# Optimization experiments

Measured on AMD Instinct MI355X. Metric: run time of the kernel, lower is better.

The kernel has to match this reference:

```python
import jax, jax.numpy as jnp
import numpy as np

N_NODES = 20000
N_EDGES = 640000
IN_DIM = 128
HID_DIM = 256
N_CLASSES = 3
N_TYPES = 4
N_ASPECTS = 4096


def _type_aware_gcn(x, W_type, W_self, b, src, dst, etypes, n_nodes):
    # Per-node, per-type transforms: [N, T, H]
    xt = jnp.einsum('nd,tdh->nth', x, W_type)
    # Per-edge message: transform of source node under the edge's type. [E, H]
    msg = xt[src, etypes]
    # Degree-normalized scatter-sum into destination nodes.
    agg = jax.ops.segment_sum(msg, dst, num_segments=n_nodes)
    deg = jax.ops.segment_sum(jnp.ones((src.shape[0],), dtype=x.dtype), dst,
                              num_segments=n_nodes)
    agg = agg / jnp.clip(deg, 1.0)[:, None]
    # Self-loop transform + bias.
    return agg + x @ W_self + b


def setup_inputs() -> dict:
    key = jax.random.key(0)
    ks = jax.random.split(key, 12)
    features = jax.random.normal(ks[0], (N_NODES, IN_DIM), dtype=jnp.float32)
    edge_index = jax.random.randint(ks[1], (2, N_EDGES), 0, N_NODES)
    edge_types = jax.random.randint(ks[2], (N_EDGES,), 0, N_TYPES)
    aspect_indices = jax.random.randint(ks[3], (N_ASPECTS,), 0, N_NODES)
    s1 = 1.0 / np.sqrt(IN_DIM)
    s2 = 1.0 / np.sqrt(HID_DIM)
    W_type1 = jax.random.uniform(ks[4], (N_TYPES, IN_DIM, HID_DIM), minval=-s1, maxval=s1)
    W_self1 = jax.random.uniform(ks[5], (IN_DIM, HID_DIM), minval=-s1, maxval=s1)
    b1 = jnp.zeros((HID_DIM,), dtype=jnp.float32)
    W_type2 = jax.random.uniform(ks[6], (N_TYPES, HID_DIM, HID_DIM), minval=-s2, maxval=s2)
    W_self2 = jax.random.uniform(ks[7], (HID_DIM, HID_DIM), minval=-s2, maxval=s2)
    b2 = jnp.zeros((HID_DIM,), dtype=jnp.float32)
    W_cls = jax.random.uniform(ks[8], (HID_DIM, N_CLASSES), minval=-s2, maxval=s2)
    b_cls = jnp.zeros((N_CLASSES,), dtype=jnp.float32)
    return {
        'features': features,
        'W_type1': W_type1, 'W_self1': W_self1, 'b1': b1,
        'W_type2': W_type2, 'W_self2': W_self2, 'b2': b2,
        'W_cls': W_cls, 'b_cls': b_cls,
        'edge_index': edge_index,
        'edge_types': edge_types,
        'aspect_indices': aspect_indices,
    }


def reference(features, W_type1, W_self1, b1, W_type2, W_self2, b2,
              W_cls, b_cls, edge_index, edge_types, aspect_indices):
    n = features.shape[0]
    src, dst = edge_index[0], edge_index[1]
    h = _type_aware_gcn(features, W_type1, W_self1, b1, src, dst, edge_types, n)
    h = jax.nn.relu(h)
    # dropout: eval mode -> identity
    h = _type_aware_gcn(h, W_type2, W_self2, b2, src, dst, edge_types, n)
    aspect_embeddings = h[aspect_indices]            # [A, H]
    logits = aspect_embeddings @ W_cls + b_cls       # [A, C]
    return logits
```

## Files before the change

### kernel.cpp

```cpp
#include <hip/hip_runtime.h>

#define N_NODES   20000
#define N_EDGES   640000
#define IN_DIM    128
#define HID_DIM   256
#define N_TYPES   4
#define N_ASPECTS 4096
#define NT4       (N_NODES * N_TYPES)
#define NBUCK     157
#define BCAP      5120
#define CHUNK     2560

typedef __bf16 v8bf __attribute__((ext_vector_type(8)));
typedef float  f32x4 __attribute__((ext_vector_type(4)));
typedef float  v2f   __attribute__((ext_vector_type(2)));

static __device__ __forceinline__ float bf2f(unsigned short u) {
    return __builtin_bit_cast(float, ((unsigned int)u) << 16);
}
static __device__ __forceinline__ float bflo(unsigned int u) {
    return __builtin_bit_cast(float, u << 16);
}
static __device__ __forceinline__ float bfhi(unsigned int u) {
    return __builtin_bit_cast(float, u & 0xffff0000u);
}
static __device__ __forceinline__ unsigned short f2bf(float f) {
    unsigned int u = __builtin_bit_cast(unsigned int, f);
    u += 0x7fffu + ((u >> 16) & 1u);
    return (unsigned short)(u >> 16);
}

static __device__ __forceinline__ int local_flag(const unsigned short* w, int* red) {
    int tid = threadIdx.x;
    int c = 0;
    for (int i = tid; i < 1024; i += 256) {
        unsigned hb = (w[i] >> 8) & 0x7f;
        c += (hb >= 0x39 && hb <= 0x3D) ? 1 : 0;
    }
#pragma unroll
    for (int off = 32; off >= 1; off >>= 1) c += __shfl_down(c, off);
    if ((tid & 63) == 0) red[tid >> 6] = c;
    __syncthreads();
    int tot = red[0] + red[1] + red[2] + red[3];
    __syncthreads();
    return (tot >= 768) ? 1 : 0;
}

__global__ __launch_bounds__(256) void prepA_kernel(
        const void* __restrict__ x,
        const void* __restrict__ Ws1, const void* __restrict__ Wt1,
        const void* __restrict__ Ws2, const void* __restrict__ Wt2,
        const int* __restrict__ ei, const int* __restrict__ et,
        unsigned short* __restrict__ xc,
        unsigned int* __restrict__ xc8,
        unsigned short* __restrict__ WT1,
        unsigned short* __restrict__ WT2,
        int* __restrict__ bucket_cursor,
        unsigned int* __restrict__ breg,
        int* __restrict__ flag) {
    __shared__ __align__(16) char smem[14336];
    int b = blockIdx.x, tid = threadIdx.x;
    if (b < 250) {
        unsigned int* ord = (unsigned int*)smem;
        int* hist  = (int*)(smem + 10240);
        int* start = hist + NBUCK;
        int* cur   = start + NBUCK;
        int* gbase = cur + NBUCK;
        int* sbuf  = gbase + NBUCK;
        int e0 = b * CHUNK;
        for (int i = tid; i < NBUCK; i += 256) hist[i] = 0;
        __syncthreads();
        unsigned int pk[10];
        int bk[10];
#pragma unroll
        for (int r = 0; r < 10; r++) {
            int e = e0 + r * 256 + tid;
            int s = __builtin_nontemporal_load(ei + e);
            int d = __builtin_nontemporal_load(ei + N_EDGES + e);
            int t = __builtin_nontemporal_load(et + e);
            pk[r] = (unsigned int)s | ((unsigned int)t << 15) | ((unsigned int)d << 17);
            bk[r] = d >> 7;
            atomicAdd(&hist[bk[r]], 1);
        }
        __syncthreads();
        int v = (tid < NBUCK) ? hist[tid] : 0;
        sbuf[tid] = v;
        __syncthreads();
        for (int o = 1; o < 256; o <<= 1) {
            int t = (tid >= o) ? sbuf[tid - o] : 0;
            __syncthreads();
            sbuf[tid] += t;
            __syncthreads();
        }
        if (tid < NBUCK) { start[tid] = sbuf[tid] - v; cur[tid] = sbuf[tid] - v; }
        __syncthreads();
#pragma unroll
        for (int r = 0; r < 10; r++) {
            int p = atomicAdd(&cur[bk[r]], 1);
            ord[p] = pk[r];
        }
        __syncthreads();
        for (int bb = tid; bb < NBUCK; bb += 256)
            if (hist[bb] > 0) gbase[bb] = atomicAdd(bucket_cursor + bb, hist[bb]);
        __syncthreads();
        for (int p = tid; p < CHUNK; p += 256) {
            unsigned int e = ord[p];
            int bb = (int)(e >> 24);
            int gp = gbase[bb] + (p - start[bb]);
            if (gp < BCAP)
                __builtin_nontemporal_store(e, breg + (size_t)bb * BCAP + gp);
        }
    } else if (b < 1500) {
        int bf = local_flag((const unsigned short*)Ws1, (int*)smem);
        int idx = (b - 250) * 256 + tid;
        float f[8];
        if (bf) {
            uint4 v = reinterpret_cast<const uint4*>(x)[idx];
            reinterpret_cast<uint4*>(xc)[idx] = v;
            f[0] = bflo(v.x); f[1] = bfhi(v.x);
            f[2] = bflo(v.y); f[3] = bfhi(v.y);
            f[4] = bflo(v.z); f[5] = bfhi(v.z);
            f[6] = bflo(v.w); f[7] = bfhi(v.w);
        } else {
            const float* xf = reinterpret_cast<const float*>(x) + (size_t)idx * 8;
            unsigned short r[8] __attribute__((aligned(16)));
#pragma unroll
            for (int j = 0; j < 8; j++) { f[j] = xf[j]; r[j] = f2bf(xf[j]); }
            reinterpret_cast<uint4*>(xc)[idx] = *reinterpret_cast<const uint4*>(r);
        }
        int lo = 0, hi = 0;
        lo = __builtin_amdgcn_cvt_pk_fp8_f32(f[0], f[1], lo, false);
        lo = __builtin_amdgcn_cvt_pk_fp8_f32(f[2], f[3], lo, true);
        hi = __builtin_amdgcn_cvt_pk_fp8_f32(f[4], f[5], hi, false);
        hi = __builtin_amdgcn_cvt_pk_fp8_f32(f[6], f[7], hi, true);
        xc8[idx * 2]     = (unsigned int)lo;
        xc8[idx * 2 + 1] = (unsigned int)hi;
    } else if (b < 2140) {
        int bf = local_flag((const unsigned short*)Ws1, (int*)smem);
        int idx = (b - 1500) * 256 + tid;
        int n = idx / 640, k = idx - n * 640;
        const void* p = (k < 128) ? Ws1 : Wt1;
        size_t src = (k < 128) ? ((size_t)k * 256 + n) : ((size_t)(k - 128) * 256 + n);
        WT1[idx] = bf ? ((const unsigned short*)p)[src] : f2bf(((const float*)p)[src]);
    } else if (b < 3420) {
        int bf = local_flag((const unsigned short*)Ws1, (int*)smem);
        int idx = (b - 2140) * 256 + tid;
        int n = idx / 1280, k = idx - n * 1280;
        const void* p = (k < 256) ? Ws2 : Wt2;
        size_t src = (k < 256) ? ((size_t)k * 256 + n) : ((size_t)(k - 256) * 256 + n);
        WT2[idx] = bf ? ((const unsigned short*)p)[src] : f2bf(((const float*)p)[src]);
    } else {
        int bf = local_flag((const unsigned short*)Ws1, (int*)smem);
        if (tid == 0) *flag = bf;
    }
}

__global__ __launch_bounds__(256) void bucketB_kernel(
        const unsigned int* __restrict__ breg,
        const int* __restrict__ bucket_cursor,
        unsigned short* __restrict__ perm,
        int* __restrict__ offsets4) {
    __shared__ int cnt[512], off[512];
    __shared__ int buf[256], pscan[256];
    int b = blockIdx.x, tid = threadIdx.x;
    int cv = (tid < NBUCK) ? bucket_cursor[tid] : 0;
    if (cv > BCAP) cv = BCAP;
    buf[tid] = cv;
    __syncthreads();
    for (int o = 1; o < 256; o <<= 1) {
        int t = (tid >= o) ? buf[tid - o] : 0;
        __syncthreads();
        buf[tid] += t;
        __syncthreads();
    }
    int obase = (b > 0) ? buf[b - 1] : 0;
    if (b == 0 && tid == 0) offsets4[NT4] = buf[255];
    int Eb = bucket_cursor[b];
    if (Eb > BCAP) Eb = BCAP;
    for (int i = tid; i < 512; i += 256) cnt[i] = 0;
    __syncthreads();
    const unsigned int* reg = breg + (size_t)b * BCAP;
    for (int i = tid; i < Eb; i += 256) {
        unsigned int e = reg[i];
        int seg = (((e >> 17) & 127) << 2) | ((e >> 15) & 3);
        atomicAdd(&cnt[seg], 1);
    }
    __syncthreads();
    int pv = cnt[2 * tid] + cnt[2 * tid + 1];
    pscan[tid] = pv;
    __syncthreads();
    for (int o = 1; o < 256; o <<= 1) {
        int t = (tid >= o) ? pscan[tid - o] : 0;
        __syncthreads();
        pscan[tid] += t;
        __syncthreads();
    }
    int pexcl = pscan[tid] - pv;
    off[2 * tid]     = pexcl;
    off[2 * tid + 1] = pexcl + cnt[2 * tid];
    __syncthreads();
    for (int i = tid; i < 512; i += 256) {
        int node = b * 128 + (i >> 2);
        if (node < N_NODES) offsets4[node * 4 + (i & 3)] = obase + off[i];
    }
    __syncthreads();
    for (int i = tid; i < Eb; i += 256) {
        unsigned int e = reg[i];
        int seg = (((e >> 17) & 127) << 2) | ((e >> 15) & 3);
        int p = atomicAdd(&off[seg], 1);
        perm[obase + p] = (unsigned short)(e & 0x7fff);
    }
}

template <int D>
__global__ __launch_bounds__(256) void agg8_kernel(
        const unsigned int* __restrict__ F8,
        const int* __restrict__ offs4,
        const unsigned short* __restrict__ perm,
        unsigned short* __restrict__ AG) {
    constexpr int G = D / 8;
    constexpr int NSUB = 64 / G;
    int wave = threadIdx.x >> 6, lane = threadIdx.x & 63;
    int sg = lane / G;
    int gl = lane - sg * G;
    for (int n = blockIdx.x * 4 + wave; n < N_NODES; n += gridDim.x * 4) {
        int o0 = offs4[n * 4];
        int o4 = offs4[n * 4 + 4];
        int deg = o4 - o0;
        float inv = 1.0f / (float)(deg > 1 ? deg : 1);
        int s0 = o0;
#pragma unroll
        for (int t = 0; t < 4; t++) {
            int s1 = offs4[n * 4 + t + 1];
            float a[8];
#pragma unroll
            for (int v = 0; v < 8; v++) a[v] = 0.f;
            int j = s0;
            while (j < s1) {
                int m = s1 - j;
                if (m > 64) m = 64;
                int pw = (int)perm[j + ((lane < m) ? lane : 0)];
                int nfull = (m / (NSUB * 4)) * (NSUB * 4);
                for (int base = 0; base < nfull; base += NSUB * 4) {
                    uint2 x[4];
#pragma unroll
                    for (int l = 0; l < 4; l++) {
                        int src = __shfl(pw, base + sg * 4 + l);
                        x[l] = *reinterpret_cast<const uint2*>(F8 + (size_t)src * (D / 4) + gl * 2);
                    }
#pragma unroll
                    for (int l = 0; l < 4; l++) {
                        v2f p0 = __builtin_amdgcn_cvt_pk_f32_fp8((int)x[l].x, false);
                        v2f p1 = __builtin_amdgcn_cvt_pk_f32_fp8((int)x[l].x, true);
                        v2f p2 = __builtin_amdgcn_cvt_pk_f32_fp8((int)x[l].y, false);
                        v2f p3 = __builtin_amdgcn_cvt_pk_f32_fp8((int)x[l].y, true);
                        a[0] += p0.x; a[1] += p0.y;
                        a[2] += p1.x; a[3] += p1.y;
                        a[4] += p2.x; a[5] += p2.y;
                        a[6] += p3.x; a[7] += p3.y;
                    }
                }
                for (int k = nfull; k < m; k += NSUB) {
                    int e = k + sg;
                    int valid = (e < m);
                    int idx = valid ? e : (m - 1);
                    int src = __shfl(pw, idx);
                    uint2 x = *reinterpret_cast<const uint2*>(F8 + (size_t)src * (D / 4) + gl * 2);
                    unsigned msk = valid ? 0xffffffffu : 0u;
                    x.x &= msk; x.y &= msk;
                    v2f p0 = __builtin_amdgcn_cvt_pk_f32_fp8((int)x.x, false);
                    v2f p1 = __builtin_amdgcn_cvt_pk_f32_fp8((int)x.x, true);
                    v2f p2 = __builtin_amdgcn_cvt_pk_f32_fp8((int)x.y, false);
                    v2f p3 = __builtin_amdgcn_cvt_pk_f32_fp8((int)x.y, true);
                    a[0] += p0.x; a[1] += p0.y;
                    a[2] += p1.x; a[3] += p1.y;
                    a[4] += p2.x; a[5] += p2.y;
                    a[6] += p3.x; a[7] += p3.y;
                }
                j += m;
            }
#pragma unroll
            for (int v = 0; v < 8; v++) {
                float s = a[v];
                s += __shfl_xor(s, G);
                if (NSUB == 4) s += __shfl_xor(s, 2 * G);
                a[v] = s * inv;
            }
            if (sg == 0) {
                unsigned short r[8] __attribute__((aligned(16)));
#pragma unroll
                for (int v = 0; v < 8; v++) r[v] = f2bf(a[v]);
                *reinterpret_cast<uint4*>(AG + (size_t)n * (4 * D) + t * D + gl * 8) =
                    *reinterpret_cast<const uint4*>(r);
            }
            s0 = s1;
        }
    }
}

template <int D>
__global__ __launch_bounds__(256, 6) void gemm_kernel(
        const unsigned short* __restrict__ X,
        const unsigned short* __restrict__ AG,
        const unsigned short* __restrict__ BT,
        const void* __restrict__ bias,
        const int* __restrict__ flagp,
        unsigned short* __restrict__ C,
        unsigned char* __restrict__ C8,
        int M, int relu) {
    constexpr int K = 5 * D;
    constexpr int LDW = 72;
    __shared__ __align__(16) unsigned short As[64 * LDW];
    __shared__ __align__(16) unsigned short Bs[64 * LDW];
    int b = blockIdx.x;
    int mt = (b & 7) + 8 * (b >> 5);
    int nt = (b >> 3) & 3;
    int mtiles = (M + 63) >> 6;
    if (mt >= mtiles) return;
    int m0 = mt * 64;
    int n0 = nt * 64;
    int tid  = threadIdx.x;
    int wave = tid >> 6, lane = tid & 63;
    int wm = wave >> 1, wn = wave & 1;
    int quad = lane >> 4, l16 = lane & 15;

    f32x4 acc[2][2];
#pragma unroll
    for (int i = 0; i < 2; i++)
#pragma unroll
        for (int j = 0; j < 2; j++) acc[i][j] = (f32x4){0.f, 0.f, 0.f, 0.f};

    for (int k0 = 0; k0 < K; k0 += 64) {
        const unsigned short* base = (k0 < D) ? X : AG;
        int rs  = (k0 < D) ? D : 4 * D;
        int col = (k0 < D) ? k0 : (k0 - D);
#pragma unroll
        for (int cc = 0; cc < 2; cc++) {
            int c   = tid + cc * 256;
            int row = c >> 3;
            int c8  = c & 7;
            uint4 va = make_uint4(0u, 0u, 0u, 0u);
            int gr = m0 + row;
            if (gr < M)
                va = *reinterpret_cast<const uint4*>(base + (size_t)gr * rs + col + c8 * 8);
            *reinterpret_cast<uint4*>(&As[row * LDW + c8 * 8]) = va;
            uint4 vb = *reinterpret_cast<const uint4*>(BT + (size_t)(n0 + row) * K + k0 + c8 * 8);
            *reinterpret_cast<uint4*>(&Bs[row * LDW + c8 * 8]) = vb;
        }
        __syncthreads();
#pragma unroll
        for (int ks = 0; ks < 2; ks++) {
            v8bf af[2], bfr[2];
#pragma unroll
            for (int i = 0; i < 2; i++)
                af[i] = *reinterpret_cast<const v8bf*>(
                    &As[(wm * 32 + i * 16 + l16) * LDW + ks * 32 + quad * 8]);
#pragma unroll
            for (int j = 0; j < 2; j++)
                bfr[j] = *reinterpret_cast<const v8bf*>(
                    &Bs[(wn * 32 + j * 16 + l16) * LDW + ks * 32 + quad * 8]);
#pragma unroll
            for (int i = 0; i < 2; i++)
#pragma unroll
                for (int j = 0; j < 2; j++)
                    acc[i][j] = __builtin_amdgcn_mfma_f32_16x16x32_bf16(af[i], bfr[j], acc[i][j], 0, 0, 0);
        }
        __syncthreads();
    }
    int bf = *flagp;
#pragma unroll
    for (int i = 0; i < 2; i++) {
#pragma unroll
        for (int j = 0; j < 2; j++) {
            int col = n0 + wn * 32 + j * 16 + l16;
            float bv = bf ? bf2f(((const unsigned short*)bias)[col])
                          : ((const float*)bias)[col];
#pragma unroll
            for (int r = 0; r < 4; r++) {
                int row = m0 + wm * 32 + i * 16 + quad * 4 + r;
                if (row < M) {
                    float v = acc[i][j][r] + bv;
                    if (relu) v = fmaxf(v, 0.0f);
                    C[(size_t)row * 256 + col] = f2bf(v);
                    if (C8) {
                        int pk = __builtin_amdgcn_cvt_pk_fp8_f32(v, v, 0, false);
                        C8[(size_t)row * 256 + col] = (unsigned char)(pk & 0xff);
                    }
                }
            }
        }
    }
}

__global__ void cls_kernel(const unsigned short* __restrict__ h2,
                           const int* __restrict__ aidx,
                           const void* __restrict__ Wc,
                           const void* __restrict__ bc,
                           const int* __restrict__ flagp,
                           void* __restrict__ out) {
    int lin = blockIdx.x * blockDim.x + threadIdx.x;
    int a = lin >> 6, lane = lin & 63;
    if (a >= N_ASPECTS) return;
    int bf = *flagp;
    int node = aidx[a];
    uint2 v = *reinterpret_cast<const uint2*>(h2 + (size_t)node * 256 + lane * 4);
    float hv[4] = {bflo(v.x), bfhi(v.x), bflo(v.y), bfhi(v.y)};
    float a0 = 0.f, a1 = 0.f, a2 = 0.f;
#pragma unroll
    for (int r = 0; r < 4; r++) {
        int k = lane * 4 + r;
        float w0 = bf ? bf2f(((const unsigned short*)Wc)[k * 3 + 0]) : ((const float*)Wc)[k * 3 + 0];
        float w1 = bf ? bf2f(((const unsigned short*)Wc)[k * 3 + 1]) : ((const float*)Wc)[k * 3 + 1];
        float w2 = bf ? bf2f(((const unsigned short*)Wc)[k * 3 + 2]) : ((const float*)Wc)[k * 3 + 2];
        a0 += hv[r] * w0;
        a1 += hv[r] * w1;
        a2 += hv[r] * w2;
    }
#pragma unroll
    for (int off = 32; off >= 1; off >>= 1) {
        a0 += __shfl_down(a0, off);
        a1 += __shfl_down(a1, off);
        a2 += __shfl_down(a2, off);
    }
    if (lane == 0) {
        float b0 = bf ? bf2f(((const unsigned short*)bc)[0]) : ((const float*)bc)[0];
        float b1 = bf ? bf2f(((const unsigned short*)bc)[1]) : ((const float*)bc)[1];
        float b2 = bf ? bf2f(((const unsigned short*)bc)[2]) : ((const float*)bc)[2];
        if (bf) {
            unsigned short* o = (unsigned short*)out;
            o[a * 3 + 0] = f2bf(a0 + b0);
            o[a * 3 + 1] = f2bf(a1 + b1);
            o[a * 3 + 2] = f2bf(a2 + b2);
        } else {
            float* o = (float*)out;
            o[a * 3 + 0] = a0 + b0;
            o[a * 3 + 1] = a1 + b1;
            o[a * 3 + 2] = a2 + b2;
        }
    }
}

extern "C" void kernel_launch(void* const* d_in, const int* in_sizes, int n_in,
                              void* d_out, int out_size, void* d_ws, size_t ws_size,
                              hipStream_t stream) {
    const void* x   = d_in[0];
    const void* Wt1 = d_in[1];
    const void* Ws1 = d_in[2];
    const void* b1  = d_in[3];
    const void* Wt2 = d_in[4];
    const void* Ws2 = d_in[5];
    const void* b2  = d_in[6];
    const void* Wc  = d_in[7];
    const void* bc  = d_in[8];
    const int* ei = (const int*)d_in[9];
    const int* et = (const int*)d_in[10];
    const int* ai = (const int*)d_in[11];

    char* ws = (char*)d_ws;
    size_t off = 0;
    auto alloc = [&](size_t bytes) {
        void* p = ws + off;
        off += (bytes + 255) & ~(size_t)255;
        return p;
    };
    int*            flag          = (int*)alloc(4);
    int*            bucket_cursor = (int*)alloc((size_t)NBUCK * 4);
    int*            offsets4      = (int*)alloc((size_t)(NT4 + 1) * 4);
    unsigned int*   breg          = (unsigned int*)alloc((size_t)NBUCK * BCAP * 4);
    unsigned short* perm          = (unsigned short*)alloc((size_t)N_EDGES * 2);
    unsigned short* xc            = (unsigned short*)alloc((size_t)N_NODES * IN_DIM * 2);
    unsigned int*   xc8           = (unsigned int*)alloc((size_t)N_NODES * IN_DIM);
    unsigned short* AG            = (unsigned short*)alloc((size_t)N_NODES * 4 * HID_DIM * 2);
    unsigned short* h             = (unsigned short*)alloc((size_t)N_NODES * HID_DIM * 2);
    unsigned char*  h8            = (unsigned char*)alloc((size_t)N_NODES * HID_DIM);
    unsigned short* h2            = (unsigned short*)alloc((size_t)N_NODES * HID_DIM * 2);
    unsigned short* WT1           = (unsigned short*)alloc((size_t)640 * 256 * 2);
    unsigned short* WT2           = (unsigned short*)alloc((size_t)1280 * 256 * 2);

    hipMemsetAsync(bucket_cursor, 0, (size_t)NBUCK * 4, stream);
    prepA_kernel<<<3421, 256, 0, stream>>>(x, Ws1, Wt1, Ws2, Wt2, ei, et,
                                           xc, xc8, WT1, WT2, bucket_cursor, breg, flag);
    bucketB_kernel<<<NBUCK, 256, 0, stream>>>(breg, bucket_cursor, perm, offsets4);

    agg8_kernel<IN_DIM><<<4096, 256, 0, stream>>>(xc8, offsets4, perm, AG);
    gemm_kernel<IN_DIM><<<1280, 256, 0, stream>>>(xc, AG, WT1, b1, flag, h, h8, N_NODES, 1);
    agg8_kernel<HID_DIM><<<4096, 256, 0, stream>>>((const unsigned int*)h8, offsets4, perm, AG);
    gemm_kernel<HID_DIM><<<1280, 256, 0, stream>>>(h, AG, WT2, b2, flag, h2, nullptr, N_NODES, 0);
    cls_kernel<<<(N_ASPECTS * 64) / 256, 256, 0, stream>>>(h2, ai, Wc, bc, flag, d_out);
}
```

Before: 231.4 us.

## Enlarge GEMM tiles to 128x128 and load tiles via direct global-to-LDS

The fused GEMM now uses 128x128 output tiles, with each wave computing a 64x64 sub-tile (4x4 MFMA accumulators), so operands are reused more per LDS load. Tiles are staged with global_load_lds 16-byte direct loads instead of going through registers. Rows past M are clamped to the last row rather than zero-filled. The risks are fewer blocks (320 vs 1280), possibly too few for the number of CUs, and LDS bank conflicts from the unpadded 64-wide rows.

```diff
diff --git a/kernel.cpp b/kernel.cpp
--- a/kernel.cpp
+++ b/kernel.cpp
@@ -28,6 +28,13 @@
     unsigned int u = __builtin_bit_cast(unsigned int, f);
     u += 0x7fffu + ((u >> 16) & 1u);
     return (unsigned short)(u >> 16);
+}
+
+static __device__ __forceinline__ void gload16(const unsigned short* g, unsigned short* l) {
+    __builtin_amdgcn_global_load_lds(
+        (const __attribute__((address_space(1))) void*)g,
+        (__attribute__((address_space(3))) void*)l,
+        16, 0, 0);
 }
 
 static __device__ __forceinline__ int local_flag(const unsigned short* w, int* red) {
@@ -299,7 +306,7 @@
 }
 
 template <int D>
-__global__ __launch_bounds__(256, 6) void gemm_kernel(
+__global__ __launch_bounds__(256) void gemm_kernel(
         const unsigned short* __restrict__ X,
         const unsigned short* __restrict__ AG,
         const unsigned short* __restrict__ BT,
@@ -309,75 +316,77 @@
         unsigned char* __restrict__ C8,
         int M, int relu) {
     constexpr int K = 5 * D;
-    constexpr int LDW = 72;
-    __shared__ __align__(16) unsigned short As[64 * LDW];
-    __shared__ __align__(16) unsigned short Bs[64 * LDW];
+    __shared__ __align__(16) unsigned short As[128 * 64];
+    __shared__ __align__(16) unsigned short Bs[128 * 64];
     int b = blockIdx.x;
-    int mt = (b & 7) + 8 * (b >> 5);
-    int nt = (b >> 3) & 3;
-    int mtiles = (M + 63) >> 6;
+    int mt = (b >> 4) * 8 + (b & 7);
+    int nt = (b >> 3) & 1;
+    int mtiles = (M + 127) >> 7;
     if (mt >= mtiles) return;
-    int m0 = mt * 64;
-    int n0 = nt * 64;
+    int m0 = mt * 128;
+    int n0 = nt * 128;
     int tid  = threadIdx.x;
     int wave = tid >> 6, lane = tid & 63;
     int wm = wave >> 1, wn = wave & 1;
     int quad = lane >> 4, l16 = lane & 15;
 
-    f32x4 acc[2][2];
-#pragma unroll
-    for (int i = 0; i < 2; i++)
-#pragma unroll
-        for (int j = 0; j < 2; j++) acc[i][j] = (f32x4){0.f, 0.f, 0.f, 0.f};
+    f32x4 acc[4][4];
+#pragma unroll
+    for (int i = 0; i < 4; i++)
+#pragma unroll
+        for (int j = 0; j < 4; j++) acc[i][j] = (f32x4){0.f, 0.f, 0.f, 0.f};
 
     for (int k0 = 0; k0 < K; k0 += 64) {
-        const unsigned short* base = (k0 < D) ? X : AG;
+        const unsigned short* abase = (k0 < D) ? X : AG;
         int rs  = (k0 < D) ? D : 4 * D;
         int col = (k0 < D) ? k0 : (k0 - D);
 #pragma unroll
-        for (int cc = 0; cc < 2; cc++) {
-            int c   = tid + cc * 256;
+        for (int p = 0; p < 4; p++) {
+            int c   = p * 256 + tid;
             int row = c >> 3;
             int c8  = c & 7;
-            uint4 va = make_uint4(0u, 0u, 0u, 0u);
-            int gr = m0 + row;
-            if (gr < M)
-                va = *reinterpret_cast<const uint4*>(base + (size_t)gr * rs + col + c8 * 8);
-            *reinterpret_cast<uint4*>(&As[row * LDW + c8 * 8]) = va;
-            uint4 vb = *reinterpret_cast<const uint4*>(BT + (size_t)(n0 + row) * K + k0 + c8 * 8);
-            *reinterpret_cast<uint4*>(&Bs[row * LDW + c8 * 8]) = vb;
+            int gr  = m0 + row;
+            if (gr >= M) gr = M - 1;
+            gload16(abase + (size_t)gr * rs + col + c8 * 8, &As[c * 8]);
+        }
+#pragma unroll
+        for (int p = 0; p < 4; p++) {
+            int c   = p * 256 + tid;
+            int row = c >> 3;
+            int c8  = c & 7;
+            gload16(BT + (size_t)(n0 + row) * K + k0 + c8 * 8, &Bs[c * 8]);
         }
         __syncthreads();
 #pragma unroll
         for (int ks = 0; ks < 2; ks++) {
-            v8bf af[2], bfr[2];
-#pragma unroll
-            for (int i = 0; i < 2; i++)
+            v8bf af[4], bfr[4];
+#pragma unroll
+            for (int i = 0; i < 4; i++)
                 af[i] = *reinterpret_cast<const v8bf*>(
-                    &As[(wm * 32 + i * 16 + l16) * LDW + ks * 32 + quad * 8]);
-#pragma unroll
-            for (int j = 0; j < 2; j++)
+                    &As[(wm * 64 + i * 16 + l16) * 64 + ks * 32 + quad * 8]);
+#pragma unroll
+            for (int j = 0; j < 4; j++)
                 bfr[j] = *reinterpret_cast<const v8bf*>(
-                    &Bs[(wn * 32 + j * 16 + l16) * LDW + ks * 32 + quad * 8]);
-#pragma unroll
-            for (int i = 0; i < 2; i++)
-#pragma unroll
-                for (int j = 0; j < 2; j++)
+                    &Bs[(wn * 64 + j * 16 + l16) * 64 + ks * 32 + quad * 8]);
+#pragma unroll
+            for (int i = 0; i < 4; i++)
+#pragma unroll
+                for (int j = 0; j < 4; j++)
                     acc[i][j] = __builtin_amdgcn_mfma_f32_16x16x32_bf16(af[i], bfr[j], acc[i][j], 0, 0, 0);
         }
         __syncthreads();
     }
     int bf = *flagp;
 #pragma unroll
-    for (int i = 0; i < 2; i++) {
-#pragma unroll
-        for (int j = 0; j < 2; j++) {
-            int col = n0 + wn * 32 + j * 16 + l16;
+    for (int i = 0; i < 4; i++) {
+#pragma unroll
+        for (int j = 0; j < 4; j++) {
+            int col = n0 + wn * 64 + j * 16 + l16;
             float bv = bf ? bf2f(((const unsigned short*)bias)[col])
                           : ((const float*)bias)[col];
 #pragma unroll
             for (int r = 0; r < 4; r++) {
-                int row = m0 + wm * 32 + i * 16 + quad * 4 + r;
+                int row = m0 + wm * 64 + i * 16 + quad * 4 + r;
                 if (row < M) {
                     float v = acc[i][j][r] + bv;
                     if (relu) v = fmaxf(v, 0.0f);
@@ -483,8 +492,8 @@
     bucketB_kernel<<<NBUCK, 256, 0, stream>>>(breg, bucket_cursor, perm, offsets4);
 
     agg8_kernel<IN_DIM><<<4096, 256, 0, stream>>>(xc8, offsets4, perm, AG);
-    gemm_kernel<IN_DIM><<<1280, 256, 0, stream>>>(xc, AG, WT1, b1, flag, h, h8, N_NODES, 1);
+    gemm_kernel<IN_DIM><<<320, 256, 0, stream>>>(xc, AG, WT1, b1, flag, h, h8, N_NODES, 1);
     agg8_kernel<HID_DIM><<<4096, 256, 0, stream>>>((const unsigned int*)h8, offsets4, perm, AG);
-    gemm_kernel<HID_DIM><<<1280, 256, 0, stream>>>(h, AG, WT2, b2, flag, h2, nullptr, N_NODES, 0);
+    gemm_kernel<HID_DIM><<<320, 256, 0, stream>>>(h, AG, WT2, b2, flag, h2, nullptr, N_NODES, 0);
     cls_kernel<<<(N_ASPECTS * 64) / 256, 256, 0, stream>>>(h2, ai, Wc, bc, flag, d_out);
 }
```

Result: slower. 244.4 us (+5.6%).

## Fuse all GCN stages into one cooperative persistent kernel with grid syncs

Applied to the files above, without the earlier changes.

Wraps the prep, bucketing, both aggregation passes, both GEMMs and the classifier into one cooperative mega-kernel. Each stage runs its former blocks as virtual blocks in a grid-stride loop, and stages are separated by grid-wide syncs. The memset is replaced by an in-kernel zeroing step. The aim is to remove the launch gaps and tail effects between seven kernels plus a memset. The cost is that the fused kernel's register use and shared memory now set the occupancy for every stage, the GEMM loses its explicit occupancy hint, and each grid barrier adds its own overhead; a multi-kernel fallback is kept for when the cooperative launch fails.

```diff
diff --git a/kernel.cpp b/kernel.cpp
--- a/kernel.cpp
+++ b/kernel.cpp
@@ -1,4 +1,5 @@
 #include <hip/hip_runtime.h>
+#include <hip/hip_cooperative_groups.h>
 
 #define N_NODES   20000
 #define N_EDGES   640000
@@ -10,10 +11,28 @@
 #define NBUCK     157
 #define BCAP      5120
 #define CHUNK     2560
+#define GEMM_VB   1280
+#define CLS_VB    ((N_ASPECTS * 64) / 256)
 
 typedef __bf16 v8bf __attribute__((ext_vector_type(8)));
 typedef float  f32x4 __attribute__((ext_vector_type(4)));
 typedef float  v2f   __attribute__((ext_vector_type(2)));
+
+struct P {
+    const void *x, *Ws1, *Wt1, *Ws2, *Wt2, *b1, *b2, *Wc, *bc;
+    const int *ei, *et, *ai;
+    unsigned short *xc;
+    unsigned int *xc8;
+    unsigned short *WT1, *WT2;
+    int *bucket_cursor;
+    unsigned int *breg;
+    int *flag;
+    unsigned short *perm;
+    int *offsets4;
+    unsigned short *AG, *h, *h2;
+    unsigned char *h8;
+    void *out;
+};
 
 static __device__ __forceinline__ float bf2f(unsigned short u) {
     return __builtin_bit_cast(float, ((unsigned int)u) << 16);
@@ -46,20 +65,8 @@
     return (tot >= 768) ? 1 : 0;
 }
 
-__global__ __launch_bounds__(256) void prepA_kernel(
-        const void* __restrict__ x,
-        const void* __restrict__ Ws1, const void* __restrict__ Wt1,
-        const void* __restrict__ Ws2, const void* __restrict__ Wt2,
-        const int* __restrict__ ei, const int* __restrict__ et,
-        unsigned short* __restrict__ xc,
-        unsigned int* __restrict__ xc8,
-        unsigned short* __restrict__ WT1,
-        unsigned short* __restrict__ WT2,
-        int* __restrict__ bucket_cursor,
-        unsigned int* __restrict__ breg,
-        int* __restrict__ flag) {
-    __shared__ __align__(16) char smem[14336];
-    int b = blockIdx.x, tid = threadIdx.x;
+static __device__ void prepA_vb(const P& p, int b, char* smem) {
+    int tid = threadIdx.x;
     if (b < 250) {
         unsigned int* ord = (unsigned int*)smem;
         int* hist  = (int*)(smem + 10240);
@@ -75,9 +82,9 @@
 #pragma unroll
         for (int r = 0; r < 10; r++) {
             int e = e0 + r * 256 + tid;
-            int s = __builtin_nontemporal_load(ei + e);
-            int d = __builtin_nontemporal_load(ei + N_EDGES + e);
-            int t = __builtin_nontemporal_load(et + e);
+            int s = __builtin_nontemporal_load(p.ei + e);
+            int d = __builtin_nontemporal_load(p.ei + N_EDGES + e);
+            int t = __builtin_nontemporal_load(p.et + e);
             pk[r] = (unsigned int)s | ((unsigned int)t << 15) | ((unsigned int)d << 17);
             bk[r] = d >> 7;
             atomicAdd(&hist[bk[r]], 1);
@@ -96,74 +103,73 @@
         __syncthreads();
 #pragma unroll
         for (int r = 0; r < 10; r++) {
-            int p = atomicAdd(&cur[bk[r]], 1);
-            ord[p] = pk[r];
+            int pp = atomicAdd(&cur[bk[r]], 1);
+            ord[pp] = pk[r];
         }
         __syncthreads();
         for (int bb = tid; bb < NBUCK; bb += 256)
-            if (hist[bb] > 0) gbase[bb] = atomicAdd(bucket_cursor + bb, hist[bb]);
-        __syncthreads();
-        for (int p = tid; p < CHUNK; p += 256) {
-            unsigned int e = ord[p];
+            if (hist[bb] > 0) gbase[bb] = atomicAdd(p.bucket_cursor + bb, hist[bb]);
+        __syncthreads();
+        for (int pp = tid; pp < CHUNK; pp += 256) {
+            unsigned int e = ord[pp];
             int bb = (int)(e >> 24);
-            int gp = gbase[bb] + (p - start[bb]);
+            int gp = gbase[bb] + (pp - start[bb]);
             if (gp < BCAP)
-                __builtin_nontemporal_store(e, breg + (size_t)bb * BCAP + gp);
-        }
+                __builtin_nontemporal_store(e, p.breg + (size_t)bb * BCAP + gp);
+        }
+        __syncthreads();
     } else if (b < 1500) {
-        int bf = local_flag((const unsigned short*)Ws1, (int*)smem);
+        int bf = local_flag((const unsigned short*)p.Ws1, (int*)smem);
         int idx = (b - 250) * 256 + tid;
         float f[8];
         if (bf) {
-            uint4 v = reinterpret_cast<const uint4*>(x)[idx];
-            reinterpret_cast<uint4*>(xc)[idx] = v;
+            uint4 v = reinterpret_cast<const uint4*>(p.x)[idx];
+            reinterpret_cast<uint4*>(p.xc)[idx] = v;
             f[0] = bflo(v.x); f[1] = bfhi(v.x);
             f[2] = bflo(v.y); f[3] = bfhi(v.y);
             f[4] = bflo(v.z); f[5] = bfhi(v.z);
             f[6] = bflo(v.w); f[7] = bfhi(v.w);
         } else {
-            const float* xf = reinterpret_cast<const float*>(x) + (size_t)idx * 8;
+            const float* xf = reinterpret_cast<const float*>(p.x) + (size_t)idx * 8;
             unsigned short r[8] __attribute__((aligned(16)));
 #pragma unroll
             for (int j = 0; j < 8; j++) { f[j] = xf[j]; r[j] = f2bf(xf[j]); }
-            reinterpret_cast<uint4*>(xc)[idx] = *reinterpret_cast<const uint4*>(r);
+            reinterpret_cast<uint4*>(p.xc)[idx] = *reinterpret_cast<const uint4*>(r);
         }
         int lo = 0, hi = 0;
         lo = __builtin_amdgcn_cvt_pk_fp8_f32(f[0], f[1], lo, false);
         lo = __builtin_amdgcn_cvt_pk_fp8_f32(f[2], f[3], lo, true);
         hi = __builtin_amdgcn_cvt_pk_fp8_f32(f[4], f[5], hi, false);
         hi = __builtin_amdgcn_cvt_pk_fp8_f32(f[6], f[7], hi, true);
-        xc8[idx * 2]     = (unsigned int)lo;
-        xc8[idx * 2 + 1] = (unsigned int)hi;
+        p.xc8[idx * 2]     = (unsigned int)lo;
+        p.xc8[idx * 2 + 1] = (unsigned int)hi;
     } else if (b < 2140) {
-        int bf = local_flag((const unsigned short*)Ws1, (int*)smem);
+        int bf = local_flag((const unsigned short*)p.Ws1, (int*)smem);
         int idx = (b - 1500) * 256 + tid;
         int n = idx / 640, k = idx - n * 640;
-        const void* p = (k < 128) ? Ws1 : Wt1;
+        const void* q = (k < 128) ? p.Ws1 : p.Wt1;
         size_t src = (k < 128) ? ((size_t)k * 256 + n) : ((size_t)(k - 128) * 256 + n);
-        WT1[idx] = bf ? ((const unsigned short*)p)[src] : f2bf(((const float*)p)[src]);
+        p.WT1[idx] = bf ? ((const unsigned short*)q)[src] : f2bf(((const float*)q)[src]);
     } else if (b < 3420) {
-        int bf = local_flag((const unsigned short*)Ws1, (int*)smem);
+        int bf = local_flag((const unsigned short*)p.Ws1, (int*)smem);
         int idx = (b - 2140) * 256 + tid;
         int n = idx / 1280, k = idx - n * 1280;
-        const void* p = (k < 256) ? Ws2 : Wt2;
+        const void* q = (k < 256) ? p.Ws2 : p.Wt2;
         size_t src = (k < 256) ? ((size_t)k * 256 + n) : ((size_t)(k - 256) * 256 + n);
-        WT2[idx] = bf ? ((const unsigned short*)p)[src] : f2bf(((const float*)p)[src]);
+        p.WT2[idx] = bf ? ((const unsigned short*)q)[src] : f2bf(((const float*)q)[src]);
     } else {
-        int bf = local_flag((const unsigned short*)Ws1, (int*)smem);
-        if (tid == 0) *flag = bf;
-    }
-}
-
-__global__ __launch_bounds__(256) void bucketB_kernel(
-        const unsigned int* __restrict__ breg,
-        const int* __restrict__ bucket_cursor,
-        unsigned short* __restrict__ perm,
-        int* __restrict__ offsets4) {
-    __shared__ int cnt[512], off[512];
-    __shared__ int buf[256], pscan[256];
-    int b = blockIdx.x, tid = threadIdx.x;
-    int cv = (tid < NBUCK) ? bucket_cursor[tid] : 0;
+        int bf = local_flag((const unsigned short*)p.Ws1, (int*)smem);
+        if (tid == 0) *p.flag = bf;
+    }
+}
+
+static __device__ void bucketB_vb(const P& p, int b, char* smem) {
+    int* cnt   = (int*)smem;
+    int* off   = cnt + 512;
+    int* buf   = off + 512;
+    int* pscan = buf + 256;
+    int tid = threadIdx.x;
+    int cv = (tid < NBUCK) ? p.bucket_cursor[tid] : 0;
     if (cv > BCAP) cv = BCAP;
     buf[tid] = cv;
     __syncthreads();
@@ -174,12 +180,12 @@
         __syncthreads();
     }
     int obase = (b > 0) ? buf[b - 1] : 0;
-    if (b == 0 && tid == 0) offsets4[NT4] = buf[255];
-    int Eb = bucket_cursor[b];
+    if (b == 0 && tid == 0) p.offsets4[NT4] = buf[255];
+    int Eb = p.bucket_cursor[b];
     if (Eb > BCAP) Eb = BCAP;
     for (int i = tid; i < 512; i += 256) cnt[i] = 0;
     __syncthreads();
-    const unsigned int* reg = breg + (size_t)b * BCAP;
+    const unsigned int* reg = p.breg + (size_t)b * BCAP;
     for (int i = tid; i < Eb; i += 256) {
         unsigned int e = reg[i];
         int seg = (((e >> 17) & 127) << 2) | ((e >> 15) & 3);
@@ -201,23 +207,23 @@
     __syncthreads();
     for (int i = tid; i < 512; i += 256) {
         int node = b * 128 + (i >> 2);
-        if (node < N_NODES) offsets4[node * 4 + (i & 3)] = obase + off[i];
+        if (node < N_NODES) p.offsets4[node * 4 + (i & 3)] = obase + off[i];
     }
     __syncthreads();
     for (int i = tid; i < Eb; i += 256) {
         unsigned int e = reg[i];
         int seg = (((e >> 17) & 127) << 2) | ((e >> 15) & 3);
-        int p = atomicAdd(&off[seg], 1);
-        perm[obase + p] = (unsigned short)(e & 0x7fff);
-    }
+        int pp = atomicAdd(&off[seg], 1);
+        p.perm[obase + pp] = (unsigned short)(e & 0x7fff);
+    }
+    __syncthreads();
 }
 
 template <int D>
-__global__ __launch_bounds__(256) void agg8_kernel(
-        const unsigned int* __restrict__ F8,
-        const int* __restrict__ offs4,
-        const unsigned short* __restrict__ perm,
-        unsigned short* __restrict__ AG) {
+static __device__ void agg8_body(const unsigned int* __restrict__ F8,
+                                 const int* __restrict__ offs4,
+                                 const unsigned short* __restrict__ perm,
+                                 unsigned short* __restrict__ AG) {
     constexpr int G = D / 8;
     constexpr int NSUB = 64 / G;
     int wave = threadIdx.x >> 6, lane = threadIdx.x & 63;
@@ -242,18 +248,18 @@
                 int pw = (int)perm[j + ((lane < m) ? lane : 0)];
                 int nfull = (m / (NSUB * 4)) * (NSUB * 4);
                 for (int base = 0; base < nfull; base += NSUB * 4) {
-                    uint2 x[4];
+                    uint2 xv[4];
 #pragma unroll
                     for (int l = 0; l < 4; l++) {
                         int src = __shfl(pw, base + sg * 4 + l);
-                        x[l] = *reinterpret_cast<const uint2*>(F8 + (size_t)src * (D / 4) + gl * 2);
+                        xv[l] = *reinterpret_cast<const uint2*>(F8 + (size_t)src * (D / 4) + gl * 2);
                     }
 #pragma unroll
                     for (int l = 0; l < 4; l++) {
-                        v2f p0 = __builtin_amdgcn_cvt_pk_f32_fp8((int)x[l].x, false);
-                        v2f p1 = __builtin_amdgcn_cvt_pk_f32_fp8((int)x[l].x, true);
-                        v2f p2 = __builtin_amdgcn_cvt_pk_f32_fp8((int)x[l].y, false);
-                        v2f p3 = __builtin_amdgcn_cvt_pk_f32_fp8((int)x[l].y, true);
+                        v2f p0 = __builtin_amdgcn_cvt_pk_f32_fp8((int)xv[l].x, false);
+                        v2f p1 = __builtin_amdgcn_cvt_pk_f32_fp8((int)xv[l].x, true);
+                        v2f p2 = __builtin_amdgcn_cvt_pk_f32_fp8((int)xv[l].y, false);
+                        v2f p3 = __builtin_amdgcn_cvt_pk_f32_fp8((int)xv[l].y, true);
                         a[0] += p0.x; a[1] += p0.y;
                         a[2] += p1.x; a[3] += p1.y;
                         a[4] += p2.x; a[5] += p2.y;
@@ -265,13 +271,13 @@
                     int valid = (e < m);
                     int idx = valid ? e : (m - 1);
                     int src = __shfl(pw, idx);
-                    uint2 x = *reinterpret_cast<const uint2*>(F8 + (size_t)src * (D / 4) + gl * 2);
+                    uint2 xv = *reinterpret_cast<const uint2*>(F8 + (size_t)src * (D / 4) + gl * 2);
                     unsigned msk = valid ? 0xffffffffu : 0u;
-                    x.x &= msk; x.y &= msk;
-                    v2f p0 = __builtin_amdgcn_cvt_pk_f32_fp8((int)x.x, false);
-                    v2f p1 = __builtin_amdgcn_cvt_pk_f32_fp8((int)x.x, true);
-                    v2f p2 = __builtin_amdgcn_cvt_pk_f32_fp8((int)x.y, false);
-                    v2f p3 = __builtin_amdgcn_cvt_pk_f32_fp8((int)x.y, true);
+                    xv.x &= msk; xv.y &= msk;
+                    v2f p0 = __builtin_amdgcn_cvt_pk_f32_fp8((int)xv.x, false);
+                    v2f p1 = __builtin_amdgcn_cvt_pk_f32_fp8((int)xv.x, true);
+                    v2f p2 = __builtin_amdgcn_cvt_pk_f32_fp8((int)xv.y, false);
+                    v2f p3 = __builtin_amdgcn_cvt_pk_f32_fp8((int)xv.y, true);
                     a[0] += p0.x; a[1] += p0.y;
                     a[2] += p1.x; a[3] += p1.y;
                     a[4] += p2.x; a[5] += p2.y;
@@ -299,7 +305,7 @@
 }
 
 template <int D>
-__global__ __launch_bounds__(256, 6) void gemm_kernel(
+static __device__ void gemm_vb(char* smem,
         const unsigned short* __restrict__ X,
         const unsigned short* __restrict__ AG,
         const unsigned short* __restrict__ BT,
@@ -307,12 +313,11 @@
         const int* __restrict__ flagp,
         unsigned short* __restrict__ C,
         unsigned char* __restrict__ C8,
-        int M, int relu) {
+        int M, int relu, int b) {
     constexpr int K = 5 * D;
     constexpr int LDW = 72;
-    __shared__ __align__(16) unsigned short As[64 * LDW];
-    __shared__ __align__(16) unsigned short Bs[64 * LDW];
-    int b = blockIdx.x;
+    unsigned short* As = (unsigned short*)smem;
+    unsigned short* Bs = As + 64 * LDW;
     int mt = (b & 7) + 8 * (b >> 5);
     int nt = (b >> 3) & 3;
     int mtiles = (M + 63) >> 6;
@@ -392,26 +397,21 @@
     }
 }
 
-__global__ void cls_kernel(const unsigned short* __restrict__ h2,
-                           const int* __restrict__ aidx,
-                           const void* __restrict__ Wc,
-                           const void* __restrict__ bc,
-                           const int* __restrict__ flagp,
-                           void* __restrict__ out) {
-    int lin = blockIdx.x * blockDim.x + threadIdx.x;
+static __device__ void cls_vb(const P& p, int vb) {
+    int lin = vb * 256 + threadIdx.x;
     int a = lin >> 6, lane = lin & 63;
     if (a >= N_ASPECTS) return;
-    int bf = *flagp;
-    int node = aidx[a];
-    uint2 v = *reinterpret_cast<const uint2*>(h2 + (size_t)node * 256 + lane * 4);
+    int bf = *p.flag;
+    int node = p.ai[a];
+    uint2 v = *reinterpret_cast<const uint2*>(p.h2 + (size_t)node * 256 + lane * 4);
     float hv[4] = {bflo(v.x), bfhi(v.x), bflo(v.y), bfhi(v.y)};
     float a0 = 0.f, a1 = 0.f, a2 = 0.f;
 #pragma unroll
     for (int r = 0; r < 4; r++) {
         int k = lane * 4 + r;
-        float w0 = bf ? bf2f(((const unsigned short*)Wc)[k * 3 + 0]) : ((const float*)Wc)[k * 3 + 0];
-        float w1 = bf ? bf2f(((const unsigned short*)Wc)[k * 3 + 1]) : ((const float*)Wc)[k * 3 + 1];
-        float w2 = bf ? bf2f(((const unsigned short*)Wc)[k * 3 + 2]) : ((const float*)Wc)[k * 3 + 2];
+        float w0 = bf ? bf2f(((const unsigned short*)p.Wc)[k * 3 + 0]) : ((const float*)p.Wc)[k * 3 + 0];
+        float w1 = bf ? bf2f(((const unsigned short*)p.Wc)[k * 3 + 1]) : ((const float*)p.Wc)[k * 3 + 1];
+        float w2 = bf ? bf2f(((const unsigned short*)p.Wc)[k * 3 + 2]) : ((const float*)p.Wc)[k * 3 + 2];
         a0 += hv[r] * w0;
         a1 += hv[r] * w1;
         a2 += hv[r] * w2;
@@ -423,16 +423,16 @@
         a2 += __shfl_down(a2, off);
     }
     if (lane == 0) {
-        float b0 = bf ? bf2f(((const unsigned short*)bc)[0]) : ((const float*)bc)[0];
-        float b1 = bf ? bf2f(((const unsigned short*)bc)[1]) : ((const float*)bc)[1];
-        float b2 = bf ? bf2f(((const unsigned short*)bc)[2]) : ((const float*)bc)[2];
+        float b0 = bf ? bf2f(((const unsigned short*)p.bc)[0]) : ((const float*)p.bc)[0];
+        float b1 = bf ? bf2f(((const unsigned short*)p.bc)[1]) : ((const float*)p.bc)[1];
+        float b2 = bf ? bf2f(((const unsigned short*)p.bc)[2]) : ((const float*)p.bc)[2];
         if (bf) {
-            unsigned short* o = (unsigned short*)out;
+            unsigned short* o = (unsigned short*)p.out;
             o[a * 3 + 0] = f2bf(a0 + b0);
             o[a * 3 + 1] = f2bf(a1 + b1);
             o[a * 3 + 2] = f2bf(a2 + b2);
         } else {
-            float* o = (float*)out;
+            float* o = (float*)p.out;
             o[a * 3 + 0] = a0 + b0;
             o[a * 3 + 1] = a1 + b1;
             o[a * 3 + 2] = a2 + b2;
@@ -440,51 +440,109 @@
     }
 }
 
+__global__ __launch_bounds__(256) void mega_kernel(P p) {
+    __shared__ __align__(16) char smem[18432];
+    cooperative_groups::grid_group g = cooperative_groups::this_grid();
+    if (blockIdx.x == 0 && threadIdx.x < NBUCK) p.bucket_cursor[threadIdx.x] = 0;
+    g.sync();
+    for (int b = blockIdx.x; b < 3421; b += gridDim.x) prepA_vb(p, b, smem);
+    g.sync();
+    for (int b = blockIdx.x; b < NBUCK; b += gridDim.x) bucketB_vb(p, b, smem);
+    g.sync();
+    agg8_body<IN_DIM>(p.xc8, p.offsets4, p.perm, p.AG);
+    g.sync();
+    for (int b = blockIdx.x; b < GEMM_VB; b += gridDim.x)
+        gemm_vb<IN_DIM>(smem, p.xc, p.AG, p.WT1, p.b1, p.flag, p.h, p.h8, N_NODES, 1, b);
+    g.sync();
+    agg8_body<HID_DIM>((const unsigned int*)p.h8, p.offsets4, p.perm, p.AG);
+    g.sync();
+    for (int b = blockIdx.x; b < GEMM_VB; b += gridDim.x)
+        gemm_vb<HID_DIM>(smem, p.h, p.AG, p.WT2, p.b2, p.flag, p.h2, nullptr, N_NODES, 0, b);
+    g.sync();
+    for (int vb = blockIdx.x; vb < CLS_VB; vb += gridDim.x) cls_vb(p, vb);
+}
+
+__global__ __launch_bounds__(256) void prepA_kernel(P p) {
+    __shared__ __align__(16) char smem[14336];
+    prepA_vb(p, blockIdx.x, smem);
+}
+__global__ __launch_bounds__(256) void bucketB_kernel(P p) {
+    __shared__ __align__(16) char smem[6144];
+    bucketB_vb(p, blockIdx.x, smem);
+}
+template <int D>
+__global__ __launch_bounds__(256) void agg8_kernel(const unsigned int* F8, const int* o,
+                                                   const unsigned short* pm, unsigned short* AG) {
+    agg8_body<D>(F8, o, pm, AG);
+}
+template <int D>
+__global__ __launch_bounds__(256) void gemm_kernel(const unsigned short* X, const unsigned short* AG,
+                                                   const unsigned short* BT, const void* bias,
+                                                   const int* flagp, unsigned short* C,
+                                                   unsigned char* C8, int M, int relu) {
+    __shared__ __align__(16) char smem[18432];
+    gemm_vb<D>(smem, X, AG, BT, bias, flagp, C, C8, M, relu, blockIdx.x);
+}
+__global__ void cls_kernel(P p) { cls_vb(p, blockIdx.x); }
+
 extern "C" void kernel_launch(void* const* d_in, const int* in_sizes, int n_in,
                               void* d_out, int out_size, void* d_ws, size_t ws_size,
                               hipStream_t stream) {
-    const void* x   = d_in[0];
-    const void* Wt1 = d_in[1];
-    const void* Ws1 = d_in[2];
-    const void* b1  = d_in[3];
-    const void* Wt2 = d_in[4];
-    const void* Ws2 = d_in[5];
-    const void* b2  = d_in[6];
-    const void* Wc  = d_in[7];
-    const void* bc  = d_in[8];
-    const int* ei = (const int*)d_in[9];
-    const int* et = (const int*)d_in[10];
-    const int* ai = (const int*)d_in[11];
-
     char* ws = (char*)d_ws;
     size_t off = 0;
     auto alloc = [&](size_t bytes) {
-        void* p = ws + off;
+        void* q = ws + off;
         off += (bytes + 255) & ~(size_t)255;
-        return p;
+        return q;
     };
-    int*            flag          = (int*)alloc(4);
-    int*            bucket_cursor = (int*)alloc((size_t)NBUCK * 4);
-    int*            offsets4      = (int*)alloc((size_t)(NT4 + 1) * 4);
-    unsigned int*   breg          = (unsigned int*)alloc((size_t)NBUCK * BCAP * 4);
-    unsigned short* perm          = (unsigned short*)alloc((size_t)N_EDGES * 2);
-    unsigned short* xc            = (unsigned short*)alloc((size_t)N_NODES * IN_DIM * 2);
-    unsigned int*   xc8           = (unsigned int*)alloc((size_t)N_NODES * IN_DIM);
-    unsigned short* AG            = (unsigned short*)alloc((size_t)N_NODES * 4 * HID_DIM * 2);
-    unsigned short* h             = (unsigned short*)alloc((size_t)N_NODES * HID_DIM * 2);
-    unsigned char*  h8            = (unsigned char*)alloc((size_t)N_NODES * HID_DIM);
-    unsigned short* h2            = (unsigned short*)alloc((size_t)N_NODES * HID_DIM * 2);
-    unsigned short* WT1           = (unsigned short*)alloc((size_t)640 * 256 * 2);
-    unsigned short* WT2           = (unsigned short*)alloc((size_t)1280 * 256 * 2);
-
-    hipMemsetAsync(bucket_cursor, 0, (size_t)NBUCK * 4, stream);
-    prepA_kernel<<<3421, 256, 0, stream>>>(x, Ws1, Wt1, Ws2, Wt2, ei, et,
-                                           xc, xc8, WT1, WT2, bucket_cursor, breg, flag);
-    bucketB_kernel<<<NBUCK, 256, 0, stream>>>(breg, bucket_cursor, perm, offsets4);
-
-    agg8_kernel<IN_DIM><<<4096, 256, 0, stream>>>(xc8, offsets4, perm, AG);
-    gemm_kernel<IN_DIM><<<1280, 256, 0, stream>>>(xc, AG, WT1, b1, flag, h, h8, N_NODES, 1);
-    agg8_kernel<HID_DIM><<<4096, 256, 0, stream>>>((const unsigned int*)h8, offsets4, perm, AG);
-    gemm_kernel<HID_DIM><<<1280, 256, 0, stream>>>(h, AG, WT2, b2, flag, h2, nullptr, N_NODES, 0);
-    cls_kernel<<<(N_ASPECTS * 64) / 256, 256, 0, stream>>>(h2, ai, Wc, bc, flag, d_out);
-}
+    P p;
+    p.x   = d_in[0];  p.Wt1 = d_in[1];  p.Ws1 = d_in[2];  p.b1 = d_in[3];
+    p.Wt2 = d_in[4];  p.Ws2 = d_in[5];  p.b2  = d_in[6];
+    p.Wc  = d_in[7];  p.bc  = d_in[8];
+    p.ei  = (const int*)d_in[9];
+    p.et  = (const int*)d_in[10];
+    p.ai  = (const int*)d_in[11];
+    p.out = d_out;
+    p.flag          = (int*)alloc(4);
+    p.bucket_cursor = (int*)alloc((size_t)NBUCK * 4);
+    p.offsets4      = (int*)alloc((size_t)(NT4 + 1) * 4);
+    p.breg          = (unsigned int*)alloc((size_t)NBUCK * BCAP * 4);
+    p.perm          = (unsigned short*)alloc((size_t)N_EDGES * 2);
+    p.xc            = (unsigned short*)alloc((size_t)N_NODES * IN_DIM * 2);
+    p.xc8           = (unsigned int*)alloc((size_t)N_NODES * IN_DIM);
+    p.AG            = (unsigned short*)alloc((size_t)N_NODES * 4 * HID_DIM * 2);
+    p.h             = (unsigned short*)alloc((size_t)N_NODES * HID_DIM * 2);
+    p.h8            = (unsigned char*)alloc((size_t)N_NODES * HID_DIM);
+    p.h2            = (unsigned short*)alloc((size_t)N_NODES * HID_DIM * 2);
+    p.WT1           = (unsigned short*)alloc((size_t)640 * 256 * 2);
+    p.WT2           = (unsigned short*)alloc((size_t)1280 * 256 * 2);
+
+    static int coop_grid = 0;
+    if (coop_grid == 0) {
+        int nb = 0;
+        if (hipOccupancyMaxActiveBlocksPerMultiprocessor(&nb, (const void*)mega_kernel, 256, 0)
+                != hipSuccess || nb < 1)
+            nb = 2;
+        int gsz = nb * 256;
+        if (gsz > GEMM_VB) gsz = GEMM_VB;
+        if (gsz < 256)     gsz = 256;
+        coop_grid = gsz;
+    }
+    void* args[] = {(void*)&p};
+    hipError_t e = hipLaunchCooperativeKernel((const void*)mega_kernel,
+                                              dim3(coop_grid), dim3(256), args, 0, stream);
+    if (e != hipSuccess) {
+        (void)hipGetLastError();
+        hipMemsetAsync(p.bucket_cursor, 0, (size_t)NBUCK * 4, stream);
+        prepA_kernel<<<3421, 256, 0, stream>>>(p);
+        bucketB_kernel<<<NBUCK, 256, 0, stream>>>(p);
+        agg8_kernel<IN_DIM><<<4096, 256, 0, stream>>>(p.xc8, p.offsets4, p.perm, p.AG);
+        gemm_kernel<IN_DIM><<<GEMM_VB, 256, 0, stream>>>(p.xc, p.AG, p.WT1, p.b1, p.flag,
+                                                         p.h, p.h8, N_NODES, 1);
+        agg8_kernel<HID_DIM><<<4096, 256, 0, stream>>>((const unsigned int*)p.h8, p.offsets4,
+                                                       p.perm, p.AG);
+        gemm_kernel<HID_DIM><<<GEMM_VB, 256, 0, stream>>>(p.h, p.AG, p.WT2, p.b2, p.flag,
+                                                          p.h2, nullptr, N_NODES, 0);
+        cls_kernel<<<CLS_VB, 256, 0, stream>>>(p);
+    }
+}
```

New measurement: 779.3 us. +236.8%, slower.
